# Kernel tuning notes

Hardware: AMD Instinct MI355X
Metric: run time of the kernel (lower is better)

Reference implementation:

```python
import jax, jax.numpy as jnp
import numpy as np

N, M, C_IN, C_OUT = 16384, 8192, 128, 64
P_EDGE = 0.005  # ~41 hyperedges per vertex


def setup_inputs() -> dict:
    key = jax.random.key(0)
    k1, k2, k3, k4 = jax.random.split(key, 4)
    X = jax.random.normal(k1, (N, C_IN), dtype=jnp.float32)
    # 0/1 incidence matrix (dense realization of a sparse hypergraph)
    H = (jax.random.uniform(k2, (N, M)) < P_EDGE).astype(jnp.float32)
    W = jax.random.normal(k3, (C_OUT, C_IN), dtype=jnp.float32) / np.sqrt(C_IN)
    b = jax.random.normal(k4, (C_OUT,), dtype=jnp.float32) * 0.01
    return {"X": X, "H": H, "W": W, "b": b}


def reference(X, H, W, b):
    # theta: linear projection  (N, C_in) -> (N, C_out)
    Xt = X @ W.T + b
    # D_v^{-1/2} and D_e^{-1} with torch-style nan_to_num semantics
    dv = jnp.nan_to_num(jnp.power(H.sum(axis=1), -0.5))  # (N,)
    de = jnp.nan_to_num(jnp.power(H.sum(axis=0), -1.0))  # (M,)
    # L @ X = diag(dv) H diag(de) H^T diag(dv) @ Xt, applied as row scalings
    # (W_e is the identity in the original code)
    Y = dv[:, None] * Xt           # (N, C_out)
    Y = H.T @ Y                    # (M, C_out) gather to hyperedges
    Y = de[:, None] * Y            # (M, C_out)
    Y = H @ Y                      # (N, C_out) scatter back to vertices
    Y = dv[:, None] * Y            # (N, C_out)
    # is_last=False -> ReLU; bn=None; dropout is identity in eval mode
    return jax.nn.relu(Y)
```

## Files before the change

### kernel.cpp

```cpp
#include <hip/hip_runtime.h>
#include <hip/hip_bf16.h>
#include <stdint.h>

#define N_V   16384
#define M_E   8192
#define CIN   128
#define COUT  64
#define RCAP  128
#define CCAP  192

#define OFF_ROWCNT  0
#define OFF_COLCNT  (N_V * 4)
#define OFF_ROWLIST (OFF_COLCNT + M_E * 4)
#define OFF_COLLIST (OFF_ROWLIST + N_V * RCAP * 2)
#define OFF_YV      (OFF_COLLIST + M_E * CCAP * 2)
#define OFF_E       (OFF_YV + N_V * COUT * 4)

__global__ __launch_bounds__(256) void k_rows(
    const uint4* __restrict__ H4,
    int* __restrict__ row_cnt, unsigned short* __restrict__ row_list) {
  int wid  = threadIdx.x >> 6;
  int lane = threadIdx.x & 63;
  int n    = blockIdx.x * 4 + wid;
  const uint4* rp = H4 + (size_t)n * (M_E / 4) + lane;
  unsigned short* rl = row_list + n * RCAP;
  unsigned long long lt = (lane == 63) ? 0x7fffffffffffffffull
                                       : ((1ull << lane) - 1ull);
  int off = 0;
#pragma unroll 4
  for (int it = 0; it < (M_E / 4) / 64; ++it) {
    uint4 v = rp[it * 64];
    unsigned long long b0 = __ballot(v.x != 0u);
    unsigned long long b1 = __ballot(v.y != 0u);
    unsigned long long b2 = __ballot(v.z != 0u);
    unsigned long long b3 = __ballot(v.w != 0u);
    int t0 = __popcll(b0), t1 = __popcll(b1), t2 = __popcll(b2), t3 = __popcll(b3);
    int total = t0 + t1 + t2 + t3;
    if (total) {
      int mb = (it * 64 + lane) * 4;
      if (v.x != 0u) { int p = off + __popcll(b0 & lt);
                       if (p < RCAP) rl[p] = (unsigned short)(mb + 0); }
      if (v.y != 0u) { int p = off + t0 + __popcll(b1 & lt);
                       if (p < RCAP) rl[p] = (unsigned short)(mb + 1); }
      if (v.z != 0u) { int p = off + t0 + t1 + __popcll(b2 & lt);
                       if (p < RCAP) rl[p] = (unsigned short)(mb + 2); }
      if (v.w != 0u) { int p = off + t0 + t1 + t2 + __popcll(b3 & lt);
                       if (p < RCAP) rl[p] = (unsigned short)(mb + 3); }
      off += total;
    }
  }
  if (lane == 0) row_cnt[n] = off < RCAP ? off : RCAP;
}

__global__ __launch_bounds__(256) void k_cols(
    const int* __restrict__ row_cnt, const unsigned short* __restrict__ row_list,
    int* __restrict__ col_cnt, unsigned short* __restrict__ col_list) {
  int t    = blockIdx.x * 256 + threadIdx.x;
  int n    = t >> 7;
  int slot = t & (RCAP - 1);
  if (slot < row_cnt[n]) {
    int e  = row_list[n * RCAP + slot];
    int cp = atomicAdd(&col_cnt[e], 1);
    if (cp < CCAP) col_list[e * CCAP + cp] = (unsigned short)n;
  }
}

__global__ __launch_bounds__(256) void k_project(
    const float* __restrict__ X, const float* __restrict__ W,
    const float* __restrict__ b, const int* __restrict__ row_cnt,
    float* __restrict__ Yv) {
  int wid  = threadIdx.x >> 6;
  int lane = threadIdx.x & 63;
  int cb   = __builtin_amdgcn_readfirstlane(wid);
  int n    = blockIdx.x * 64 + lane;
  const float* xrow  = X + n * CIN;
  const float* wbase = W + cb * 16 * CIN;

  float acc[16];
#pragma unroll
  for (int j = 0; j < 16; ++j) acc[j] = 0.f;

  for (int k4 = 0; k4 < CIN / 4; ++k4) {
    float4 x = *(const float4*)(xrow + k4 * 4);
#pragma unroll
    for (int j = 0; j < 16; ++j) {
      float4 w = *(const float4*)(wbase + j * CIN + k4 * 4);
      acc[j] += x.x * w.x + x.y * w.y + x.z * w.z + x.w * w.w;
    }
  }

  int cnt  = row_cnt[n];
  float dv = cnt > 0 ? rsqrtf((float)cnt) : 0.f;
  float* yrow = Yv + n * COUT + cb * 16;
#pragma unroll
  for (int g = 0; g < 4; ++g) {
    float4 o;
    o.x = dv * (acc[4 * g + 0] + b[cb * 16 + 4 * g + 0]);
    o.y = dv * (acc[4 * g + 1] + b[cb * 16 + 4 * g + 1]);
    o.z = dv * (acc[4 * g + 2] + b[cb * 16 + 4 * g + 2]);
    o.w = dv * (acc[4 * g + 3] + b[cb * 16 + 4 * g + 3]);
    *(float4*)(yrow + 4 * g) = o;
  }
}

__global__ __launch_bounds__(256) void k_edge(
    const float* __restrict__ Yv, const int* __restrict__ col_cnt,
    const unsigned short* __restrict__ col_list, float* __restrict__ E) {
  int wid  = threadIdx.x >> 6;
  int lane = threadIdx.x & 63;
  int m    = blockIdx.x * 4 + wid;
  int cnt  = col_cnt[m];
  if (cnt > CCAP) cnt = CCAP;
  const unsigned short* lst = col_list + m * CCAP;
  float acc = 0.f;
  int i = 0;
  for (; i + 8 <= cnt; i += 8) {
    uint4 u = *(const uint4*)(lst + i);
    int n0 = u.x & 0xffff, n1 = u.x >> 16;
    int n2 = u.y & 0xffff, n3 = u.y >> 16;
    int n4 = u.z & 0xffff, n5 = u.z >> 16;
    int n6 = u.w & 0xffff, n7 = u.w >> 16;
    float a0 = Yv[n0 * COUT + lane];
    float a1 = Yv[n1 * COUT + lane];
    float a2 = Yv[n2 * COUT + lane];
    float a3 = Yv[n3 * COUT + lane];
    float a4 = Yv[n4 * COUT + lane];
    float a5 = Yv[n5 * COUT + lane];
    float a6 = Yv[n6 * COUT + lane];
    float a7 = Yv[n7 * COUT + lane];
    acc += ((a0 + a1) + (a2 + a3)) + ((a4 + a5) + (a6 + a7));
  }
  for (; i < cnt; ++i) acc += Yv[(int)lst[i] * COUT + lane];
  int realcnt = col_cnt[m];
  float den = realcnt > 0 ? 1.f / (float)realcnt : 0.f;
  E[m * COUT + lane] = den * acc;
}

__global__ __launch_bounds__(256) void k_vertex(
    const float* __restrict__ E, const int* __restrict__ row_cnt,
    const unsigned short* __restrict__ row_list, float* __restrict__ out) {
  int wid  = threadIdx.x >> 6;
  int lane = threadIdx.x & 63;
  int n    = blockIdx.x * 4 + wid;
  int cnt  = row_cnt[n];
  const unsigned short* lst = row_list + n * RCAP;
  float acc = 0.f;
  int i = 0;
  for (; i + 8 <= cnt; i += 8) {
    uint4 u = *(const uint4*)(lst + i);
    int m0 = u.x & 0xffff, m1 = u.x >> 16;
    int m2 = u.y & 0xffff, m3 = u.y >> 16;
    int m4 = u.z & 0xffff, m5 = u.z >> 16;
    int m6 = u.w & 0xffff, m7 = u.w >> 16;
    float a0 = E[m0 * COUT + lane];
    float a1 = E[m1 * COUT + lane];
    float a2 = E[m2 * COUT + lane];
    float a3 = E[m3 * COUT + lane];
    float a4 = E[m4 * COUT + lane];
    float a5 = E[m5 * COUT + lane];
    float a6 = E[m6 * COUT + lane];
    float a7 = E[m7 * COUT + lane];
    acc += ((a0 + a1) + (a2 + a3)) + ((a4 + a5) + (a6 + a7));
  }
  for (; i < cnt; ++i) acc += E[(int)lst[i] * COUT + lane];
  float dv = cnt > 0 ? rsqrtf((float)cnt) : 0.f;
  out[n * COUT + lane] = fmaxf(dv * acc, 0.f);
}

extern "C" void kernel_launch(void* const* d_in, const int* in_sizes, int n_in,
                              void* d_out, int out_size, void* d_ws, size_t ws_size,
                              hipStream_t stream) {
  const float* X = (const float*)d_in[0];
  const float* H = (const float*)d_in[1];
  const float* W = (const float*)d_in[2];
  const float* b = (const float*)d_in[3];
  float* out = (float*)d_out;

  char* ws = (char*)d_ws;
  int* row_cnt = (int*)(ws + OFF_ROWCNT);
  int* col_cnt = (int*)(ws + OFF_COLCNT);
  unsigned short* row_list = (unsigned short*)(ws + OFF_ROWLIST);
  unsigned short* col_list = (unsigned short*)(ws + OFF_COLLIST);
  float* Yv = (float*)(ws + OFF_YV);
  float* E  = (float*)(ws + OFF_E);

  hipMemsetAsync(col_cnt, 0, M_E * 4, stream);

  k_rows<<<N_V / 4, 256, 0, stream>>>((const uint4*)H, row_cnt, row_list);
  k_cols<<<N_V * RCAP / 256, 256, 0, stream>>>(row_cnt, row_list, col_cnt, col_list);
  k_project<<<N_V / 64, 256, 0, stream>>>(X, W, b, row_cnt, Yv);
  k_edge<<<M_E / 4, 256, 0, stream>>>(Yv, col_cnt, col_list, E);
  k_vertex<<<N_V / 4, 256, 0, stream>>>(E, row_cnt, row_list, out);
}
```

Baseline: 753.4 us.

## Replace global-atomic column transpose with chunked LDS histogram, scan and fill

The incidence transpose that built per-hyperedge vertex lists with one global atomicAdd per nonzero is replaced by three kernels. The first builds per-chunk histograms in LDS, the second does an exclusive scan over chunks per hyperedge, and the third fills the lists using LDS atomics from the scanned offsets. This removes contended global atomics and the memset, and makes column lists roughly ordered by vertex, which may help gather locality. The trade-off is that only 64 blocks run the hist and fill kernels, each thread walking its row serially, so parallelism is low; the row-scan loop is also unrolled further.

New measurement: 754.1 us. No clear change (+0.1%).

```diff
diff --git a/kernel.cpp b/kernel.cpp
--- a/kernel.cpp
+++ b/kernel.cpp
@@ -8,6 +8,8 @@
 #define COUT  64
 #define RCAP  128
 #define CCAP  192
+#define CHUNKS 64
+#define RPC   (N_V / CHUNKS)
 
 #define OFF_ROWCNT  0
 #define OFF_COLCNT  (N_V * 4)
@@ -15,6 +17,7 @@
 #define OFF_COLLIST (OFF_ROWLIST + N_V * RCAP * 2)
 #define OFF_YV      (OFF_COLLIST + M_E * CCAP * 2)
 #define OFF_E       (OFF_YV + N_V * COUT * 4)
+#define OFF_HIST    (OFF_E + M_E * COUT * 4)
 
 __global__ __launch_bounds__(256) void k_rows(
     const uint4* __restrict__ H4,
@@ -24,10 +27,9 @@
   int n    = blockIdx.x * 4 + wid;
   const uint4* rp = H4 + (size_t)n * (M_E / 4) + lane;
   unsigned short* rl = row_list + n * RCAP;
-  unsigned long long lt = (lane == 63) ? 0x7fffffffffffffffull
-                                       : ((1ull << lane) - 1ull);
+  unsigned long long lt = (1ull << lane) - 1ull;
   int off = 0;
-#pragma unroll 4
+#pragma unroll 8
   for (int it = 0; it < (M_E / 4) / 64; ++it) {
     uint4 v = rp[it * 64];
     unsigned long long b0 = __ballot(v.x != 0u);
@@ -52,16 +54,48 @@
   if (lane == 0) row_cnt[n] = off < RCAP ? off : RCAP;
 }
 
-__global__ __launch_bounds__(256) void k_cols(
+__global__ __launch_bounds__(256) void k_hist(
     const int* __restrict__ row_cnt, const unsigned short* __restrict__ row_list,
-    int* __restrict__ col_cnt, unsigned short* __restrict__ col_list) {
-  int t    = blockIdx.x * 256 + threadIdx.x;
-  int n    = t >> 7;
-  int slot = t & (RCAP - 1);
-  if (slot < row_cnt[n]) {
-    int e  = row_list[n * RCAP + slot];
-    int cp = atomicAdd(&col_cnt[e], 1);
-    if (cp < CCAP) col_list[e * CCAP + cp] = (unsigned short)n;
+    unsigned int* __restrict__ hist) {
+  __shared__ unsigned int h[M_E];
+  for (int i = threadIdx.x; i < M_E; i += 256) h[i] = 0u;
+  __syncthreads();
+  int n = blockIdx.x * RPC + threadIdx.x;
+  int cnt = row_cnt[n];
+  const unsigned short* lst = row_list + n * RCAP;
+  for (int i = 0; i < cnt; ++i) atomicAdd(&h[lst[i]], 1u);
+  __syncthreads();
+  unsigned int* out = hist + (size_t)blockIdx.x * M_E;
+  for (int i = threadIdx.x; i < M_E; i += 256) out[i] = h[i];
+}
+
+__global__ __launch_bounds__(256) void k_scan(
+    unsigned int* __restrict__ hist, int* __restrict__ col_cnt) {
+  int e = blockIdx.x * 256 + threadIdx.x;
+  unsigned int run = 0;
+#pragma unroll 8
+  for (int c = 0; c < CHUNKS; ++c) {
+    unsigned int hv = hist[(size_t)c * M_E + e];
+    hist[(size_t)c * M_E + e] = run;
+    run += hv;
+  }
+  col_cnt[e] = (int)run;
+}
+
+__global__ __launch_bounds__(256) void k_fill(
+    const int* __restrict__ row_cnt, const unsigned short* __restrict__ row_list,
+    const unsigned int* __restrict__ hist, unsigned short* __restrict__ col_list) {
+  __shared__ unsigned int h[M_E];
+  const unsigned int* base = hist + (size_t)blockIdx.x * M_E;
+  for (int i = threadIdx.x; i < M_E; i += 256) h[i] = base[i];
+  __syncthreads();
+  int n = blockIdx.x * RPC + threadIdx.x;
+  int cnt = row_cnt[n];
+  const unsigned short* lst = row_list + n * RCAP;
+  for (int i = 0; i < cnt; ++i) {
+    int e = lst[i];
+    unsigned int slot = atomicAdd(&h[e], 1u);
+    if (slot < CCAP) col_list[e * CCAP + slot] = (unsigned short)n;
   }
 }
 
@@ -109,8 +143,8 @@
   int wid  = threadIdx.x >> 6;
   int lane = threadIdx.x & 63;
   int m    = blockIdx.x * 4 + wid;
-  int cnt  = col_cnt[m];
-  if (cnt > CCAP) cnt = CCAP;
+  int realcnt = col_cnt[m];
+  int cnt  = realcnt > CCAP ? CCAP : realcnt;
   const unsigned short* lst = col_list + m * CCAP;
   float acc = 0.f;
   int i = 0;
@@ -131,7 +165,6 @@
     acc += ((a0 + a1) + (a2 + a3)) + ((a4 + a5) + (a6 + a7));
   }
   for (; i < cnt; ++i) acc += Yv[(int)lst[i] * COUT + lane];
-  int realcnt = col_cnt[m];
   float den = realcnt > 0 ? 1.f / (float)realcnt : 0.f;
   E[m * COUT + lane] = den * acc;
 }
@@ -183,11 +216,12 @@
   unsigned short* col_list = (unsigned short*)(ws + OFF_COLLIST);
   float* Yv = (float*)(ws + OFF_YV);
   float* E  = (float*)(ws + OFF_E);
-
-  hipMemsetAsync(col_cnt, 0, M_E * 4, stream);
+  unsigned int* hist = (unsigned int*)(ws + OFF_HIST);
 
   k_rows<<<N_V / 4, 256, 0, stream>>>((const uint4*)H, row_cnt, row_list);
-  k_cols<<<N_V * RCAP / 256, 256, 0, stream>>>(row_cnt, row_list, col_cnt, col_list);
+  k_hist<<<CHUNKS, 256, 0, stream>>>(row_cnt, row_list, hist);
+  k_scan<<<M_E / 256, 256, 0, stream>>>(hist, col_cnt);
+  k_fill<<<CHUNKS, 256, 0, stream>>>(row_cnt, row_list, hist, col_list);
   k_project<<<N_V / 64, 256, 0, stream>>>(X, W, b, row_cnt, Yv);
   k_edge<<<M_E / 4, 256, 0, stream>>>(Yv, col_cnt, col_list, E);
   k_vertex<<<N_V / 4, 256, 0, stream>>>(E, row_cnt, row_list, out);
```
